# Optimization experiments

Hardware: AMD Instinct MI355X
Metric: run time of the kernel (lower is better)

Reference implementation:

```python
import jax, jax.numpy as jnp
import numpy as np

D_MODEL = 1024
DIM_K = 128
DIM_V = 128

def setup_inputs() -> dict:
    key = jax.random.key(0)
    ks = jax.random.split(key, 8)
    B, T = 4, 2048
    s = 1.0 / np.sqrt(D_MODEL)
    return {
        "X_Q": jax.random.normal(ks[0], (B, T, D_MODEL), jnp.float32),
        "X_KV": jax.random.normal(ks[1], (B, T, D_MODEL), jnp.float32),
        "Wq": jax.random.normal(ks[2], (D_MODEL, DIM_K), jnp.float32) * s,
        "bq": jnp.zeros((DIM_K,), jnp.float32),
        "Wk": jax.random.normal(ks[3], (D_MODEL, DIM_K), jnp.float32) * s,
        "bk": jnp.zeros((DIM_K,), jnp.float32),
        "Wv": jax.random.normal(ks[4], (D_MODEL, DIM_V), jnp.float32) * s,
        "bv": jnp.zeros((DIM_V,), jnp.float32),
    }

def reference(X_Q, X_KV, Wq, bq, Wk, bk, Wv, bv):
    T = X_Q.shape[1]
    Q = X_Q @ Wq + bq                      # [B, T, dk]
    K = X_KV @ Wk + bk                     # [B, T, dk]
    V = X_KV @ Wv + bv                     # [B, T, dv]
    scale = 1.0 / jnp.sqrt(jnp.float32(DIM_K))
    scores = jnp.einsum('bqd,bkd->bqk', Q, K) * scale  # [B, T, T]
    causal = jnp.tril(jnp.ones((T, T), bool))
    scores = jnp.where(causal, scores, -jnp.inf)
    attn = jax.nn.softmax(scores, axis=-1)
    return jnp.einsum('bqk,bkd->bqd', attn, V)         # [B, T, dv]
```

## Files before the change

### kernel.cpp

```cpp
#include <hip/hip_runtime.h>
#include <hip/hip_bf16.h>
#include <math.h>

#define BT 8192
#define TT 2048
#define DM 1024
#define DK 128
#define NBLK 65

typedef __bf16 bf16x8 __attribute__((ext_vector_type(8)));
typedef float  f32x4  __attribute__((ext_vector_type(4)));
typedef unsigned short ushort4v __attribute__((ext_vector_type(4)));
typedef unsigned short ushort8v __attribute__((ext_vector_type(8)));

static __device__ __forceinline__ unsigned short f2bf(float x) {
    union { float f; unsigned u; } v; v.f = x;
    unsigned r = v.u + 0x7fffu + ((v.u >> 16) & 1u);
    return (unsigned short)(r >> 16);
}
static __device__ __forceinline__ float bf2f(unsigned short u) {
    union { unsigned u; float f; } v; v.u = (unsigned)u << 16;
    return v.f;
}

__host__ __device__ constexpr int slc_of(int q) { return (q == 0) ? 1 : ((q + 1) >> 1); }
__host__ __device__ constexpr int pfx_of(int q) { return (q == 0) ? 0 : 1 + (q * q - (q & 1)) / 4; }

#define QSCALE 0.1275312772629451f

__global__ __launch_bounds__(256) void wt_prep(
    const float* __restrict__ Wq, const float* __restrict__ Wk,
    const float* __restrict__ Wv, unsigned short* __restrict__ Wt)
{
    const int z = blockIdx.y;
    const float* __restrict__ W = (z == 0) ? Wq : (z == 1 ? Wk : Wv);
    const int k0 = blockIdx.x * 64;

    __shared__ __align__(16) __bf16 T[128][72];
    const int t = threadIdx.x;

#pragma unroll
    for (int jj = 0; jj < 8; ++jj) {
        int c  = jj * 256 + t;
        int k  = c >> 5;
        int n4 = (c & 31) * 4;
        float4 f = *reinterpret_cast<const float4*>(&W[(size_t)(k0 + k) * DK + n4]);
        T[n4 + 0][k] = (__bf16)f.x;
        T[n4 + 1][k] = (__bf16)f.y;
        T[n4 + 2][k] = (__bf16)f.z;
        T[n4 + 3][k] = (__bf16)f.w;
    }
    __syncthreads();

    const int n  = t >> 1;
    const int cb = (t & 1) * 32;
#pragma unroll
    for (int jj = 0; jj < 4; ++jj) {
        *reinterpret_cast<ushort8v*>(&Wt[((size_t)z * DK + n) * DM + k0 + cb + jj * 8]) =
            *reinterpret_cast<const ushort8v*>(&T[n][cb + jj * 8]);
    }
}

__global__ __launch_bounds__(256, 4) void proj_mfma(
    const float* __restrict__ XQ, const float* __restrict__ XKV,
    const unsigned short* __restrict__ Wt,
    const float* __restrict__ bq, const float* __restrict__ bk,
    const float* __restrict__ bv,
    unsigned short* __restrict__ Qb, unsigned short* __restrict__ Kb,
    unsigned short* __restrict__ Vt)
{
    const int z = blockIdx.y;
    const float* __restrict__ X    = (z == 0) ? XQ : XKV;
    const float* __restrict__ bias = (z == 0) ? bq : (z == 1 ? bk : bv);
    const unsigned short* __restrict__ Wz = Wt + (size_t)z * DK * DM;

    __shared__ __align__(16) __bf16 Wl[2][128][72];

    const int t    = threadIdx.x;
    const int lane = t & 63;
    const int wv   = t >> 6;
    const int i16  = lane & 15;
    const int g    = lane >> 4;
    const int m0   = blockIdx.x * 64;

    const float* __restrict__ Xrow =
        X + (size_t)(m0 + wv * 16 + i16) * DM + g * 8;
    const unsigned short* __restrict__ Wrow =
        Wz + (size_t)(t >> 1) * DM + (t & 1) * 32;

    f32x4 acc[8];
#pragma unroll
    for (int nt = 0; nt < 8; ++nt) acc[nt] = (f32x4){0.f, 0.f, 0.f, 0.f};

    float4   xa[4], xb[4];
    ushort8v wr_[4];

#define LOADX(xr_, k0_)                                                        \
    {                                                                          \
        _Pragma("unroll")                                                      \
        for (int c = 0; c < 2; ++c)                                            \
            _Pragma("unroll")                                                  \
            for (int h = 0; h < 2; ++h)                                        \
                xr_[c * 2 + h] = *reinterpret_cast<const float4*>(             \
                    &Xrow[(k0_) + c * 32 + h * 4]);                            \
    }
#define LOADW(k0_)                                                             \
    {                                                                          \
        _Pragma("unroll")                                                      \
        for (int i = 0; i < 4; ++i)                                            \
            wr_[i] = *reinterpret_cast<const ushort8v*>(&Wrow[(k0_) + i * 8]); \
    }
#define WRITEW(buf_)                                                           \
    {                                                                          \
        _Pragma("unroll")                                                      \
        for (int i = 0; i < 4; ++i)                                            \
            *reinterpret_cast<ushort8v*>(                                      \
                &Wl[buf_][t >> 1][(t & 1) * 32 + i * 8]) = wr_[i];             \
    }
#define COMPUTE(xr_, buf_)                                                     \
    {                                                                          \
        _Pragma("unroll")                                                      \
        for (int c = 0; c < 2; ++c) {                                          \
            union { __bf16 b[8]; bf16x8 v; } u;                                \
            u.b[0] = (__bf16)xr_[c * 2].x;  u.b[1] = (__bf16)xr_[c * 2].y;     \
            u.b[2] = (__bf16)xr_[c * 2].z;  u.b[3] = (__bf16)xr_[c * 2].w;     \
            u.b[4] = (__bf16)xr_[c * 2 + 1].x; u.b[5] = (__bf16)xr_[c * 2 + 1].y; \
            u.b[6] = (__bf16)xr_[c * 2 + 1].z; u.b[7] = (__bf16)xr_[c * 2 + 1].w; \
            _Pragma("unroll")                                                  \
            for (int nt = 0; nt < 8; ++nt) {                                   \
                bf16x8 wf = *reinterpret_cast<const bf16x8*>(                  \
                    &Wl[buf_][nt * 16 + i16][c * 32 + g * 8]);                 \
                acc[nt] = __builtin_amdgcn_mfma_f32_16x16x32_bf16(u.v, wf, acc[nt], 0, 0, 0); \
            }                                                                  \
        }                                                                      \
    }

    LOADX(xa, 0);
    LOADW(0);
    WRITEW(0);
    __syncthreads();
    LOADW(64);
    LOADX(xb, 64);

#pragma unroll
    for (int t2 = 0; t2 < 16; t2 += 2) {
        COMPUTE(xa, 0);
        WRITEW(1);
        __syncthreads();
        if (t2 + 2 < 16) { LOADW((t2 + 2) * 64); LOADX(xa, (t2 + 2) * 64); }
        COMPUTE(xb, 1);
        if (t2 + 3 < 16) WRITEW(0);
        __syncthreads();
        if (t2 + 3 < 16) { LOADW((t2 + 3) * 64); LOADX(xb, (t2 + 3) * 64); }
    }
#undef LOADX
#undef LOADW
#undef WRITEW
#undef COMPUTE

    if (z == 0) {
#pragma unroll
        for (int nt = 0; nt < 8; ++nt) {
            int n = nt * 16 + i16;
            float bb = bias[n];
#pragma unroll
            for (int r = 0; r < 4; ++r) {
                int mrow = m0 + wv * 16 + g * 4 + r;
                Qb[(size_t)mrow * DK + n] = f2bf((acc[nt][r] + bb) * QSCALE);
            }
        }
    } else if (z == 1) {
#pragma unroll
        for (int nt = 0; nt < 8; ++nt) {
            int n = nt * 16 + i16;
            float bb = bias[n];
#pragma unroll
            for (int r = 0; r < 4; ++r) {
                int mrow = m0 + wv * 16 + g * 4 + r;
                Kb[(size_t)mrow * DK + n] = f2bf(acc[nt][r] + bb);
            }
        }
    } else {
        const int b  = m0 / TT;
        const int t0 = (m0 % TT) + wv * 16 + g * 4;
#pragma unroll
        for (int nt = 0; nt < 8; ++nt) {
            int d = nt * 16 + i16;
            float bb = bias[d];
            ushort4v r;
#pragma unroll
            for (int e = 0; e < 4; ++e) r[e] = f2bf(acc[nt][e] + bb);
            *reinterpret_cast<ushort4v*>(&Vt[((size_t)b * DK + d) * TT + t0]) = r;
        }
    }
}

__global__ __launch_bounds__(512, 2) void attn_kernel(
    const unsigned short* __restrict__ Qb, const unsigned short* __restrict__ Kb,
    const unsigned short* __restrict__ Vt,
    unsigned short* __restrict__ pO, float* __restrict__ pMS)
{
    __shared__ __align__(16) unsigned short lds_[2][16384];

    const int t    = threadIdx.x;
    const int lane = t & 63;
    const int w    = t >> 6;
    const int qi   = lane & 15;
    const int g    = lane >> 4;

    const int bi    = blockIdx.x;
    const int batch = bi / NBLK;
    const int rr    = bi - batch * NBLK;
    int qbl = 0;
#pragma unroll
    for (int i = 1; i < 16; ++i) if (rr >= pfx_of(i)) qbl = i;
    const int slice = rr - (qbl == 0 ? 0 : 1 + (qbl * qbl - (qbl & 1)) / 4);
    const int S     = (qbl == 0) ? 1 : ((qbl + 1) >> 1);
    const int nch   = 2 * qbl + 2;
    const int q0    = qbl * 128;

    const unsigned short* __restrict__ Kbb = Kb + (size_t)batch * TT * DK;
    const unsigned short* __restrict__ Vtb = Vt + (size_t)batch * DK * TT;

    const int qrow  = q0 + w * 16 + qi;
    const int qminw = q0 + w * 16;
    const int qmaxw = q0 + w * 16 + 15;

    bf16x8 qf[4];
#pragma unroll
    for (int c = 0; c < 4; ++c)
        qf[c] = *reinterpret_cast<const bf16x8*>(
            &Qb[((size_t)batch * TT + qrow) * DK + c * 32 + g * 8]);

    f32x4 accO[8];
#pragma unroll
    for (int dt = 0; dt < 8; ++dt) accO[dt] = (f32x4){0.f, 0.f, 0.f, 0.f};
    float m = -1e30f, s = 0.f;

    ushort8v sreg[4];
    const int kslot0 = (w & 3) * 256;

#define STAGE_ISSUE(c_)                                                         \
    {                                                                           \
        const int k0s = (c_) * 64;                                              \
        if (w < 4) {                                                            \
            _Pragma("unroll")                                                   \
            for (int i = 0; i < 4; ++i) {                                       \
                int slot = kslot0 + i * 64 + lane;                              \
                int row  = slot >> 4;                                           \
                int colg = (slot & 15) ^ (row & 15);                            \
                sreg[i] = *reinterpret_cast<const ushort8v*>(                   \
                    &Kbb[(size_t)(k0s + row) * DK + colg * 8]);                 \
            }                                                                   \
        } else {                                                                \
            _Pragma("unroll")                                                   \
            for (int i = 0; i < 4; ++i) {                                       \
                int slot = kslot0 + i * 64 + lane;                              \
                int row  = slot >> 3;                                           \
                int colg = (slot & 7) ^ (row & 7);                              \
                sreg[i] = *reinterpret_cast<const ushort8v*>(                   \
                    &Vtb[(size_t)row * TT + k0s + colg * 8]);                   \
            }                                                                   \
        }                                                                       \
    }

#define STAGE_WRITE(buf_)                                                       \
    {                                                                           \
        const int base = (w < 4) ? 0 : 8192;                                    \
        _Pragma("unroll")                                                       \
        for (int i = 0; i < 4; ++i) {                                           \
            int slot = kslot0 + i * 64 + lane;                                  \
            *reinterpret_cast<ushort8v*>(&lds_[buf_][base + slot * 8]) = sreg[i]; \
        }                                                                       \
    }

    STAGE_ISSUE(slice);
    STAGE_WRITE(0);
    __syncthreads();

    int buf = 0;
    for (int c = slice; c < nch; c += S) {
        const int cn = c + S;
        if (cn < nch) STAGE_ISSUE(cn);

        const int k0 = c * 64;
        if (k0 <= qmaxw) {
            f32x4 accS[4];
#pragma unroll
            for (int ks = 0; ks < 4; ++ks) accS[ks] = (f32x4){0.f, 0.f, 0.f, 0.f};
#pragma unroll
            for (int cc = 0; cc < 4; ++cc) {
#pragma unroll
                for (int ks = 0; ks < 4; ++ks) {
                    bf16x8 kf = *reinterpret_cast<const bf16x8*>(
                        &lds_[buf][(ks * 16 + qi) * 128 + ((cc * 4 + g) ^ qi) * 8]);
                    accS[ks] = __builtin_amdgcn_mfma_f32_16x16x32_bf16(kf, qf[cc], accS[ks], 0, 0, 0);
                }
            }

            float xmax = -1e30f;
            if (k0 + 63 > qminw) {
#pragma unroll
                for (int ks = 0; ks < 4; ++ks)
#pragma unroll
                    for (int r = 0; r < 4; ++r) {
                        int k = k0 + ks * 16 + g * 4 + r;
                        float v0 = (k <= qrow) ? accS[ks][r] : -1e30f;
                        accS[ks][r] = v0;
                        xmax = fmaxf(xmax, v0);
                    }
            } else {
#pragma unroll
                for (int ks = 0; ks < 4; ++ks)
#pragma unroll
                    for (int r = 0; r < 4; ++r) xmax = fmaxf(xmax, accS[ks][r]);
            }

            if (__any(xmax > m + 8.f)) {
                xmax = fmaxf(xmax, __shfl_xor(xmax, 16));
                xmax = fmaxf(xmax, __shfl_xor(xmax, 32));
                float mn   = fmaxf(m, xmax);
                float corr = __builtin_amdgcn_exp2f(m - mn);
                s *= corr;
#pragma unroll
                for (int dt = 0; dt < 8; ++dt)
#pragma unroll
                    for (int e = 0; e < 4; ++e) accO[dt][e] *= corr;
                m = mn;
            }

            unsigned pk[8];
#pragma unroll
            for (int ks = 0; ks < 4; ++ks)
#pragma unroll
                for (int h = 0; h < 2; ++h) {
                    float plo = __builtin_amdgcn_exp2f(accS[ks][h * 2]     - m);
                    float phi = __builtin_amdgcn_exp2f(accS[ks][h * 2 + 1] - m);
                    s += plo + phi;
                    pk[ks * 2 + h] = (unsigned)f2bf(plo) | ((unsigned)f2bf(phi) << 16);
                }

            const int srcl0 = qi + 32 * (g & 1);
            bf16x8 pf[2];
#pragma unroll
            for (int c2 = 0; c2 < 2; ++c2) {
                union { unsigned u[4]; bf16x8 v; } pu;
#pragma unroll
                for (int w4 = 0; w4 < 4; ++w4) {
                    int srcl = srcl0 + 16 * (w4 >> 1);
                    int a = __shfl((int)pk[c2 * 4 + (w4 & 1)],     srcl);
                    int b = __shfl((int)pk[c2 * 4 + 2 + (w4 & 1)], srcl);
                    pu.u[w4] = (g & 2) ? (unsigned)b : (unsigned)a;
                }
                pf[c2] = pu.v;
            }

#pragma unroll
            for (int dt = 0; dt < 8; ++dt) {
#pragma unroll
                for (int c2 = 0; c2 < 2; ++c2) {
                    bf16x8 vf = *reinterpret_cast<const bf16x8*>(
                        &lds_[buf][8192 + (dt * 16 + qi) * 64 + ((c2 * 4 + g) ^ (qi & 7)) * 8]);
                    accO[dt] = __builtin_amdgcn_mfma_f32_16x16x32_bf16(vf, pf[c2], accO[dt], 0, 0, 0);
                }
            }
        }

        if (cn < nch) STAGE_WRITE(buf ^ 1);
        __syncthreads();
        buf ^= 1;
    }

    float srow = s + __shfl_xor(s, 16);
    srow += __shfl_xor(srow, 32);

    const size_t prow = (size_t)bi * 128 + w * 16 + qi;
    if (g == 0) {
        pMS[prow * 2]     = m;
        pMS[prow * 2 + 1] = srow;
    }
#pragma unroll
    for (int dt = 0; dt < 8; ++dt) {
        ushort4v r;
#pragma unroll
        for (int e = 0; e < 4; ++e) r[e] = f2bf(accO[dt][e]);
        *reinterpret_cast<ushort4v*>(&pO[prow * DK + dt * 16 + g * 4]) = r;
    }
#undef STAGE_ISSUE
#undef STAGE_WRITE
}

__global__ __launch_bounds__(256) void attn_combine(
    const unsigned short* __restrict__ pO, const float* __restrict__ pMS,
    float* __restrict__ O)
{
    const int t  = threadIdx.x;
    const int r  = blockIdx.x * 8 + (t >> 5);
    const int dq = (t & 31) * 4;

    const int batch = r >> 11;
    const int qbl   = (r >> 7) & 15;
    const int lr    = r & 127;
    const int S     = (qbl == 0) ? 1 : ((qbl + 1) >> 1);
    const int base  = batch * NBLK + (qbl == 0 ? 0 : 1 + (qbl * qbl - (qbl & 1)) / 4);

    float mstar = -1e30f;
    for (int ss = 0; ss < S; ++ss)
        mstar = fmaxf(mstar, pMS[((size_t)(base + ss) * 128 + lr) * 2]);

    float den = 0.f;
    float num[4] = {0.f, 0.f, 0.f, 0.f};
    for (int ss = 0; ss < S; ++ss) {
        const size_t pr = (size_t)(base + ss) * 128 + lr;
        float ms = pMS[pr * 2];
        float sv = pMS[pr * 2 + 1];
        float wgt = __builtin_amdgcn_exp2f(ms - mstar);
        den += wgt * sv;
        ushort4v ov = *reinterpret_cast<const ushort4v*>(&pO[pr * DK + dq]);
#pragma unroll
        for (int e = 0; e < 4; ++e) num[e] += wgt * bf2f(ov[e]);
    }

    const float inv = 1.f / den;
    float4 out;
    out.x = num[0] * inv; out.y = num[1] * inv;
    out.z = num[2] * inv; out.w = num[3] * inv;
    *reinterpret_cast<float4*>(&O[(size_t)r * DK + dq]) = out;
}

extern "C" void kernel_launch(void* const* d_in, const int* in_sizes, int n_in,
                              void* d_out, int out_size, void* d_ws, size_t ws_size,
                              hipStream_t stream) {
    const float* XQ  = (const float*)d_in[0];
    const float* XKV = (const float*)d_in[1];
    const float* Wq  = (const float*)d_in[2];
    const float* bq  = (const float*)d_in[3];
    const float* Wk  = (const float*)d_in[4];
    const float* bk  = (const float*)d_in[5];
    const float* Wv  = (const float*)d_in[6];
    const float* bv  = (const float*)d_in[7];

    unsigned short* Qb = (unsigned short*)d_ws;
    unsigned short* Kb = Qb + (size_t)BT * DK;
    unsigned short* Vt = Kb + (size_t)BT * DK;
    unsigned short* Wt = Vt + (size_t)BT * DK;
    float*          pMS = (float*)(Wt + (size_t)3 * DK * DM);
    unsigned short* pO  = (unsigned short*)(pMS + (size_t)4 * NBLK * 128 * 2);

    wt_prep<<<dim3(16, 3), 256, 0, stream>>>(Wq, Wk, Wv, Wt);

    proj_mfma<<<dim3(BT / 64, 3), 256, 0, stream>>>(
        XQ, XKV, Wt, bq, bk, bv, Qb, Kb, Vt);

    attn_kernel<<<dim3(4 * NBLK), 512, 0, stream>>>(Qb, Kb, Vt, pO, pMS);

    attn_combine<<<dim3(BT / 8), 256, 0, stream>>>(pO, pMS, (float*)d_out);
}
```

Baseline: 61.66 us.

## Stage projection X and W tiles via direct global-to-LDS loads with XOR swizzle

Replaces the register-staged loads of X (fp32) and W (bf16) in the projection GEMM with __builtin_amdgcn_global_load_lds DMA into a double-buffered LDS area, using XOR-swizzled layouts to avoid bank conflicts. X now lives in LDS as fp32 and is converted to bf16 at compute time. The change removes register pressure and VGPR round trips, and drops the occupancy hint from launch_bounds. In exchange it uses 64KB of LDS per block, which may limit occupancy. Synchronisation relies on __syncthreads covering the async LDS loads.

Result: no change. 60.89 us (-1.3%).

```diff
diff --git a/kernel.cpp b/kernel.cpp
--- a/kernel.cpp
+++ b/kernel.cpp
@@ -61,7 +61,7 @@
     }
 }
 
-__global__ __launch_bounds__(256, 4) void proj_mfma(
+__global__ __launch_bounds__(256) void proj_mfma(
     const float* __restrict__ XQ, const float* __restrict__ XKV,
     const unsigned short* __restrict__ Wt,
     const float* __restrict__ bq, const float* __restrict__ bk,
@@ -74,7 +74,7 @@
     const float* __restrict__ bias = (z == 0) ? bq : (z == 1 ? bk : bv);
     const unsigned short* __restrict__ Wz = Wt + (size_t)z * DK * DM;
 
-    __shared__ __align__(16) __bf16 Wl[2][128][72];
+    __shared__ __align__(16) unsigned char lds_[2][32768];
 
     const int t    = threadIdx.x;
     const int lane = t & 63;
@@ -83,79 +83,81 @@
     const int g    = lane >> 4;
     const int m0   = blockIdx.x * 64;
 
-    const float* __restrict__ Xrow =
-        X + (size_t)(m0 + wv * 16 + i16) * DM + g * 8;
-    const unsigned short* __restrict__ Wrow =
-        Wz + (size_t)(t >> 1) * DM + (t & 1) * 32;
-
     f32x4 acc[8];
 #pragma unroll
     for (int nt = 0; nt < 8; ++nt) acc[nt] = (f32x4){0.f, 0.f, 0.f, 0.f};
 
-    float4   xa[4], xb[4];
-    ushort8v wr_[4];
-
-#define LOADX(xr_, k0_)                                                        \
+#define GLOADX(buf_, kk_)                                                      \
     {                                                                          \
         _Pragma("unroll")                                                      \
-        for (int c = 0; c < 2; ++c)                                            \
-            _Pragma("unroll")                                                  \
-            for (int h = 0; h < 2; ++h)                                        \
-                xr_[c * 2 + h] = *reinterpret_cast<const float4*>(             \
-                    &Xrow[(k0_) + c * 32 + h * 4]);                            \
-    }
-#define LOADW(k0_)                                                             \
+        for (int j = 0; j < 4; ++j) {                                          \
+            const int s    = (wv * 4 + j) * 1024 + lane * 16;                  \
+            const int row  = s >> 8;             \
+            const int gran = (s >> 4) & 15;                                    \
+            const float* gp = X + (size_t)(m0 + row) * DM + (kk_) * 64         \
+                              + ((gran ^ (row & 15)) << 2);                    \
+            __builtin_amdgcn_global_load_lds(                                  \
+                (const unsigned int*)gp,                                       \
+                (unsigned int*)&lds_[buf_][(wv * 4 + j) * 1024], 16, 0, 0);    \
+        }                                                                      \
+    }
+#define GLOADW(buf_, kk_)                                                      \
     {                                                                          \
         _Pragma("unroll")                                                      \
-        for (int i = 0; i < 4; ++i)                                            \
-            wr_[i] = *reinterpret_cast<const ushort8v*>(&Wrow[(k0_) + i * 8]); \
-    }
-#define WRITEW(buf_)                                                           \
+        for (int j = 0; j < 4; ++j) {                                          \
+            const int s    = (wv * 4 + j) * 1024 + lane * 16;                  \
+            const int row  = s >> 7;             \
+            const int gran = (s >> 4) & 7;                                     \
+            const unsigned short* gp = Wz + (size_t)row * DM + (kk_) * 64      \
+                              + ((gran ^ (row & 7)) << 3);                     \
+            __builtin_amdgcn_global_load_lds(                                  \
+                (const unsigned int*)gp,                                       \
+                (unsigned int*)&lds_[buf_][16384 + (wv * 4 + j) * 1024],       \
+                16, 0, 0);                                                     \
+        }                                                                      \
+    }
+#define COMPUTE(buf_)                                                          \
     {                                                                          \
-        _Pragma("unroll")                                                      \
-        for (int i = 0; i < 4; ++i)                                            \
-            *reinterpret_cast<ushort8v*>(                                      \
-                &Wl[buf_][t >> 1][(t & 1) * 32 + i * 8]) = wr_[i];             \
-    }
-#define COMPUTE(xr_, buf_)                                                     \
-    {                                                                          \
+        const float*  Xl = (const float*)&lds_[buf_][0];                       \
+        const __bf16* Wl = (const __bf16*)&lds_[buf_][16384];                  \
         _Pragma("unroll")                                                      \
         for (int c = 0; c < 2; ++c) {                                          \
+            const int r   = wv * 16 + i16;                                     \
+            const int gr0 = 8 * c + 2 * g;                                     \
+            float4 x0 = *reinterpret_cast<const float4*>(                      \
+                Xl + r * 64 + ((gr0 ^ (r & 15)) << 2));                        \
+            float4 x1 = *reinterpret_cast<const float4*>(                      \
+                Xl + r * 64 + (((gr0 + 1) ^ (r & 15)) << 2));                  \
             union { __bf16 b[8]; bf16x8 v; } u;                                \
-            u.b[0] = (__bf16)xr_[c * 2].x;  u.b[1] = (__bf16)xr_[c * 2].y;     \
-            u.b[2] = (__bf16)xr_[c * 2].z;  u.b[3] = (__bf16)xr_[c * 2].w;     \
-            u.b[4] = (__bf16)xr_[c * 2 + 1].x; u.b[5] = (__bf16)xr_[c * 2 + 1].y; \
-            u.b[6] = (__bf16)xr_[c * 2 + 1].z; u.b[7] = (__bf16)xr_[c * 2 + 1].w; \
+            u.b[0] = (__bf16)x0.x; u.b[1] = (__bf16)x0.y;                      \
+            u.b[2] = (__bf16)x0.z; u.b[3] = (__bf16)x0.w;                      \
+            u.b[4] = (__bf16)x1.x; u.b[5] = (__bf16)x1.y;                      \
+            u.b[6] = (__bf16)x1.z; u.b[7] = (__bf16)x1.w;                      \
             _Pragma("unroll")                                                  \
             for (int nt = 0; nt < 8; ++nt) {                                   \
+                const int wr = nt * 16 + i16;                                  \
                 bf16x8 wf = *reinterpret_cast<const bf16x8*>(                  \
-                    &Wl[buf_][nt * 16 + i16][c * 32 + g * 8]);                 \
-                acc[nt] = __builtin_amdgcn_mfma_f32_16x16x32_bf16(u.v, wf, acc[nt], 0, 0, 0); \
+                    Wl + wr * 64 + (((4 * c + g) ^ (wr & 7)) << 3));           \
+                acc[nt] = __builtin_amdgcn_mfma_f32_16x16x32_bf16(             \
+                    u.v, wf, acc[nt], 0, 0, 0);                                \
             }                                                                  \
         }                                                                      \
     }
 
-    LOADX(xa, 0);
-    LOADW(0);
-    WRITEW(0);
+    GLOADX(0, 0); GLOADW(0, 0);
     __syncthreads();
-    LOADW(64);
-    LOADX(xb, 64);
-
-#pragma unroll
-    for (int t2 = 0; t2 < 16; t2 += 2) {
-        COMPUTE(xa, 0);
-        WRITEW(1);
+
+#pragma unroll
+    for (int kk = 0; kk < 16; kk += 2) {
+        GLOADX(1, kk + 1); GLOADW(1, kk + 1);
+        COMPUTE(0);
         __syncthreads();
-        if (t2 + 2 < 16) { LOADW((t2 + 2) * 64); LOADX(xa, (t2 + 2) * 64); }
-        COMPUTE(xb, 1);
-        if (t2 + 3 < 16) WRITEW(0);
+        if (kk + 2 < 16) { GLOADX(0, kk + 2); GLOADW(0, kk + 2); }
+        COMPUTE(1);
         __syncthreads();
-        if (t2 + 3 < 16) { LOADW((t2 + 3) * 64); LOADX(xb, (t2 + 3) * 64); }
-    }
-#undef LOADX
-#undef LOADW
-#undef WRITEW
+    }
+#undef GLOADX
+#undef GLOADW
 #undef COMPUTE
 
     if (z == 0) {
```
